# Optimization experiments

Hardware: AMD Instinct MI355X
Metric: run time of the kernel (lower is better)

## Reference

```python
import jax, jax.numpy as jnp
import numpy as np

N = 50000      # nodes
E = 400000     # edges
D = 512        # embed_dim
L = 3          # num gcn layers
INNER = (L + 1) * D
EPS = 1e-5     # BatchNorm1d eps


def setup_inputs() -> dict:
    key = jax.random.key(0)
    ks = jax.random.split(key, 6)
    x = jax.random.normal(ks[0], (N, D), dtype=jnp.float32)
    edge_index = jax.random.randint(ks[1], (2, E), 0, N, dtype=jnp.int64)
    Ws = jax.random.normal(ks[2], (L, D, D), dtype=jnp.float32) / np.float32(np.sqrt(D))
    bs = jnp.zeros((L, D), jnp.float32)
    bn_gamma = jnp.ones((INNER,), jnp.float32)
    bn_beta = jnp.zeros((INNER,), jnp.float32)
    out_W = jax.random.normal(ks[3], (INNER, D), dtype=jnp.float32) / np.float32(np.sqrt(INNER))
    out_b = jnp.zeros((D,), jnp.float32)
    return {"x": x, "edge_index": edge_index, "Ws": Ws, "bs": bs,
            "bn_gamma": bn_gamma, "bn_beta": bn_beta, "out_W": out_W, "out_b": out_b}


def _gcn_conv(x, W, b, src, dst):
    # PyG GCNConv: add self-loops, sym-normalize, aggregate source->target.
    h = x @ W                                            # [N, D]
    deg = jnp.zeros((N,), x.dtype).at[dst].add(1.0) + 1.0  # in-degree + self-loop
    dinv = jax.lax.rsqrt(deg)
    norm = dinv[src] * dinv[dst]                         # [E]
    agg = jnp.zeros_like(h).at[dst].add(h[src] * norm[:, None])
    agg = agg + h * (dinv * dinv)[:, None]               # self-loop messages
    return agg + b


def reference(x, edge_index, Ws, bs, bn_gamma, bn_beta, out_W, out_b):
    src, dst = edge_index[0], edge_index[1]
    h = x
    x_cat = [x]
    for l in range(L):                                   # fixed small layer loop
        h = jax.nn.gelu(_gcn_conv(h, Ws[l], bs[l], src, dst), approximate=False)
        x_cat.append(h)
    xc = jnp.concatenate(x_cat, axis=-1)                 # [N, (L+1)*D]
    # BatchNorm1d, training-mode batch statistics (biased variance)
    mean = jnp.mean(xc, axis=0)
    var = jnp.var(xc, axis=0)
    xn = (xc - mean) * jax.lax.rsqrt(var + EPS) * bn_gamma + bn_beta
    return xn @ out_W + out_b                            # [N, D]
```

## Files before the change

### kernel.cpp

```cpp
#include <hip/hip_runtime.h>
#include <math.h>

#define N_NODES 50000
#define N_EDGES 400000
#define DIM 512
#define NLAYER 3
#define INNER 2048
#define BN_EPS 1e-5f
#define MPAD 50048

typedef unsigned short u16;
typedef unsigned int u32;

typedef __attribute__((ext_vector_type(8))) short bf16x8;
typedef __attribute__((ext_vector_type(4))) float f32x4;

__device__ __forceinline__ u16 f2bf(float f) {
  union { float f; u32 u; } v; v.f = f;
  u32 u = v.u;
  u32 r = (u + 0x7FFFu + ((u >> 16) & 1u)) >> 16;
  return (u16)r;
}
__device__ __forceinline__ float bf2f(u16 h) {
  union { u32 u; float f; } v; v.u = ((u32)h) << 16; return v.f;
}

#define GLOAD_LDS16(g, l)                                                       \
  __builtin_amdgcn_global_load_lds(                                             \
      (const __attribute__((address_space(1))) u32*)(g),                        \
      (__attribute__((address_space(3))) u32*)(l), 16, 0, 0)


__global__ void k_deg(const int* __restrict__ ei, int* __restrict__ deg) {
  int e = blockIdx.x * blockDim.x + threadIdx.x;
  if (e < N_EDGES) atomicAdd(&deg[ei[N_EDGES + e]], 1);
}

__global__ void k_dinv(const int* __restrict__ deg, float* __restrict__ dinv) {
  int i = blockIdx.x * blockDim.x + threadIdx.x;
  if (i < N_NODES) dinv[i] = rsqrtf((float)(deg[i] + 1));
}

__global__ __launch_bounds__(1024) void k_scan(const int* __restrict__ deg,
                                               int* __restrict__ offs, int n) {
  __shared__ int wsum[16];
  __shared__ int carry;
  int tid = threadIdx.x;
  int lane = tid & 63, wv = tid >> 6;
  if (tid == 0) carry = 0;
  __syncthreads();
  for (int base = 0; base < n; base += 1024) {
    int i = base + tid;
    int v = (i < n) ? deg[i] : 0;
    int x = v;
#pragma unroll
    for (int d = 1; d < 64; d <<= 1) {
      int y = __shfl_up(x, d, 64);
      if (lane >= d) x += y;
    }
    if (lane == 63) wsum[wv] = x;
    __syncthreads();
    if (wv == 0) {
      int w = (lane < 16) ? wsum[lane] : 0;
#pragma unroll
      for (int d = 1; d < 16; d <<= 1) {
        int y = __shfl_up(w, d, 64);
        if (lane >= d) w += y;
      }
      if (lane < 16) wsum[lane] = w;
    }
    __syncthreads();
    int prev = carry + (wv ? wsum[wv - 1] : 0);
    if (i < n) offs[i] = prev + x - v;
    int total = wsum[15];
    __syncthreads();
    if (tid == 0) carry += total;
    __syncthreads();
  }
  if (tid == 0) offs[n] = carry;
}

__global__ void k_fill(const int* __restrict__ ei, const int* __restrict__ offs,
                       int* __restrict__ cursor, const float* __restrict__ dinv,
                       int* __restrict__ csr_src, float* __restrict__ csr_norm) {
  int e = blockIdx.x * blockDim.x + threadIdx.x;
  if (e >= N_EDGES) return;
  int s = ei[e];
  int d = ei[N_EDGES + e];
  int p = atomicAdd(&cursor[d], 1);
  int idx = offs[d] + p;
  csr_src[idx] = s;
  csr_norm[idx] = dinv[s] * dinv[d];
}

__global__ void k_convert(const float* __restrict__ src, u16* __restrict__ dst, int n4) {
  int i = blockIdx.x * blockDim.x + threadIdx.x;
  if (i >= n4) return;
  float4 v = ((const float4*)src)[i];
  uint2 o;
  o.x = (u32)f2bf(v.x) | ((u32)f2bf(v.y) << 16);
  o.y = (u32)f2bf(v.z) | ((u32)f2bf(v.w) << 16);
  ((uint2*)dst)[i] = o;
}

__global__ void k_transpose_scale(const float* __restrict__ W, const float* __restrict__ scale,
                                  u16* __restrict__ WT, int K) {
  int t = blockIdx.x * blockDim.x + threadIdx.x;
  if (t >= K * DIM) return;
  int k = t >> 9;
  int j = t & 511;
  float v = W[t];
  if (scale) v *= scale[k];
  WT[(size_t)j * K + k] = f2bf(v);
}

#define BM 128
#define BN 128
#define BK 32

__global__ __launch_bounds__(256) void gemm_bt(
    const u16* __restrict__ A0, const u16* __restrict__ A1,
    const u16* __restrict__ A2, const u16* __restrict__ A3,
    const u16* __restrict__ Bt, const float* __restrict__ bias,
    float* __restrict__ Cf, u16* __restrict__ Cb, int M, int K) {
  __shared__ __align__(16) u16 As[BM * BK];
  __shared__ __align__(16) u16 Bs[BN * BK];
  int tid = threadIdx.x;
  int n0 = blockIdx.x * BN;
  int m0 = blockIdx.y * BM;
  int wave = tid >> 6, lane = tid & 63;
  int wm = (wave & 1) * 64, wn = (wave >> 1) * 64;
  int lr = lane & 15;
  int lq = lane >> 4;

  int ric = lane >> 2;
  int seg = (lane & 3) * 8;

  f32x4 acc[4][4];
#pragma unroll
  for (int i = 0; i < 4; i++)
#pragma unroll
    for (int j = 0; j < 4; j++) acc[i][j] = (f32x4){0.f, 0.f, 0.f, 0.f};

  for (int k0 = 0; k0 < K; k0 += BK) {
    int b = k0 >> 9;
    int kcol = k0 & 511;
    const u16* Abase = (b == 0) ? A0 : (b == 1) ? A1 : (b == 2) ? A2 : A3;
#pragma unroll
    for (int c = 0; c < 2; c++) {
      int chunk = wave * 2 + c;
      int arow = chunk * 16 + ric;
      GLOAD_LDS16(Abase + (size_t)(m0 + arow) * DIM + kcol + seg, &As[chunk * 512]);
      GLOAD_LDS16(Bt + (size_t)(n0 + arow) * K + k0 + seg, &Bs[chunk * 512]);
    }
    __syncthreads();
    bf16x8 af[4], bfr[4];
#pragma unroll
    for (int i = 0; i < 4; i++)
      af[i] = *(const bf16x8*)(&As[(wm + i * 16 + lr) * BK + lq * 8]);
#pragma unroll
    for (int j = 0; j < 4; j++)
      bfr[j] = *(const bf16x8*)(&Bs[(wn + j * 16 + lr) * BK + lq * 8]);
#pragma unroll
    for (int i = 0; i < 4; i++)
#pragma unroll
      for (int j = 0; j < 4; j++)
        acc[i][j] = __builtin_amdgcn_mfma_f32_16x16x32_bf16(af[i], bfr[j], acc[i][j], 0, 0, 0);
    __syncthreads();
  }
#pragma unroll
  for (int i = 0; i < 4; i++) {
    int row_b = m0 + wm + i * 16 + lq * 4;
#pragma unroll
    for (int j = 0; j < 4; j++) {
      int col = n0 + wn + j * 16 + lr;
      float bv = bias ? bias[col] : 0.f;
#pragma unroll
      for (int r = 0; r < 4; r++) {
        int row = row_b + r;
        if (row < M) {
          if (Cf) Cf[(size_t)row * DIM + col] = acc[i][j][r] + bv;
          else    Cb[(size_t)row * DIM + col] = f2bf(acc[i][j][r]);
        }
      }
    }
  }
}

__global__ __launch_bounds__(128) void k_aggregate(
    const u16* __restrict__ hp, const int* __restrict__ offs,
    const int* __restrict__ csr_src, const float* __restrict__ csr_norm,
    const float* __restrict__ dinv, const float* __restrict__ b,
    u16* __restrict__ hb_out) {
  int v = blockIdx.x;
  int c4 = threadIdx.x * 4;
  float4 acc = {0.f, 0.f, 0.f, 0.f};
  int e0 = offs[v], e1 = offs[v + 1];
  for (int e = e0; e < e1; e++) {
    int s = csr_src[e];
    float w = csr_norm[e];
    uint2 hv = *(const uint2*)(hp + (size_t)s * DIM + c4);
    acc.x += w * bf2f((u16)(hv.x & 0xffffu));
    acc.y += w * bf2f((u16)(hv.x >> 16));
    acc.z += w * bf2f((u16)(hv.y & 0xffffu));
    acc.w += w * bf2f((u16)(hv.y >> 16));
  }
  float di = dinv[v];
  float w2 = di * di;
  uint2 hv = *(const uint2*)(hp + (size_t)v * DIM + c4);
  float4 bb = *(const float4*)(b + c4);
  acc.x += w2 * bf2f((u16)(hv.x & 0xffffu)) + bb.x;
  acc.y += w2 * bf2f((u16)(hv.x >> 16)) + bb.y;
  acc.z += w2 * bf2f((u16)(hv.y & 0xffffu)) + bb.z;
  acc.w += w2 * bf2f((u16)(hv.y >> 16)) + bb.w;
  acc.x = 0.5f * acc.x * (1.f + erff(acc.x * 0.70710678118654752f));
  acc.y = 0.5f * acc.y * (1.f + erff(acc.y * 0.70710678118654752f));
  acc.z = 0.5f * acc.z * (1.f + erff(acc.z * 0.70710678118654752f));
  acc.w = 0.5f * acc.w * (1.f + erff(acc.w * 0.70710678118654752f));
  uint2 o;
  o.x = (u32)f2bf(acc.x) | ((u32)f2bf(acc.y) << 16);
  o.y = (u32)f2bf(acc.z) | ((u32)f2bf(acc.w) << 16);
  *(uint2*)(hb_out + (size_t)v * DIM + c4) = o;
}

__global__ void k_bn_stats(const u16* __restrict__ b0, const u16* __restrict__ b1,
                           const u16* __restrict__ b2, const u16* __restrict__ b3,
                           float* __restrict__ sums, float* __restrict__ sumsq,
                           int rows_per) {
  const u16* buf = (blockIdx.x == 0) ? b0 : (blockIdx.x == 1) ? b1 : (blockIdx.x == 2) ? b2 : b3;
  int c = threadIdx.x * 2;
  int col = blockIdx.x * DIM + c;
  int r0 = blockIdx.y * rows_per;
  int r1 = min(N_NODES, r0 + rows_per);
  float s0 = 0.f, ss0 = 0.f, s1 = 0.f, ss1 = 0.f;
  for (int r = r0; r < r1; r++) {
    u32 u = *(const u32*)(buf + (size_t)r * DIM + c);
    float x0 = bf2f((u16)(u & 0xffffu));
    float x1 = bf2f((u16)(u >> 16));
    s0 += x0; ss0 += x0 * x0;
    s1 += x1; ss1 += x1 * x1;
  }
  atomicAdd(&sums[col], s0);
  atomicAdd(&sumsq[col], ss0);
  atomicAdd(&sums[col + 1], s1);
  atomicAdd(&sumsq[col + 1], ss1);
}

__global__ void k_bn_finalize(const float* __restrict__ sums, const float* __restrict__ sumsq,
                              const float* __restrict__ gamma, const float* __restrict__ beta,
                              float* __restrict__ scale, float* __restrict__ shift) {
  int c = blockIdx.x * blockDim.x + threadIdx.x;
  if (c >= INNER) return;
  float mean = sums[c] / (float)N_NODES;
  float var = sumsq[c] / (float)N_NODES - mean * mean;
  float rstd = rsqrtf(var + BN_EPS);
  float sc = gamma[c] * rstd;
  scale[c] = sc;
  shift[c] = beta[c] - mean * sc;
}

__global__ void k_fold_bias(const float* __restrict__ outW, const float* __restrict__ shift,
                            const float* __restrict__ outb, float* __restrict__ biasp) {
  int j = blockIdx.x * blockDim.x + threadIdx.x;
  if (j >= DIM) return;
  float s = 0.f;
  for (int k = 0; k < INNER; k++) s += shift[k] * outW[(size_t)k * DIM + j];
  biasp[j] = s + outb[j];
}

extern "C" void kernel_launch(void* const* d_in, const int* in_sizes, int n_in,
                              void* d_out, int out_size, void* d_ws, size_t ws_size,
                              hipStream_t stream) {
  (void)in_sizes; (void)n_in; (void)out_size; (void)ws_size;
  const float* x     = (const float*)d_in[0];
  const int*   ei    = (const int*)d_in[1];
  const float* Ws    = (const float*)d_in[2];
  const float* bs    = (const float*)d_in[3];
  const float* gamma = (const float*)d_in[4];
  const float* beta  = (const float*)d_in[5];
  const float* outW  = (const float*)d_in[6];
  const float* outb  = (const float*)d_in[7];
  float* out = (float*)d_out;
  u16*   hp  = (u16*)d_out;

  char* ws = (char*)d_ws;
  size_t off = 0;
  auto alloc = [&](size_t bytes) -> void* {
    void* p = ws + off;
    off = (off + bytes + 255) & ~(size_t)255;
    return p;
  };
  int*   deg    = (int*)alloc(N_NODES * 4);
  int*   cursor = (int*)alloc(N_NODES * 4);
  float* sums   = (float*)alloc(INNER * 4);
  float* sumsq  = (float*)alloc(INNER * 4);
  size_t zero_bytes = off;
  float* dinv     = (float*)alloc(N_NODES * 4);
  int*   offs     = (int*)alloc((N_NODES + 1) * 4);
  int*   csr_src  = (int*)alloc(N_EDGES * 4);
  float* csr_norm = (float*)alloc(N_EDGES * 4);
  u16*   xb  = (u16*)alloc((size_t)MPAD * DIM * 2);
  u16*   hb1 = (u16*)alloc((size_t)MPAD * DIM * 2);
  u16*   hb2 = (u16*)alloc((size_t)MPAD * DIM * 2);
  u16*   hb3 = (u16*)alloc((size_t)MPAD * DIM * 2);
  u16*   WbT = (u16*)alloc((size_t)DIM * DIM * 2);
  u16*   WpT = (u16*)alloc((size_t)INNER * DIM * 2);
  float* scale = (float*)alloc(INNER * 4);
  float* shift = (float*)alloc(INNER * 4);
  float* biasp = (float*)alloc(DIM * 4);

  hipMemsetAsync(d_ws, 0, zero_bytes, stream);
  k_deg<<<(N_EDGES + 255) / 256, 256, 0, stream>>>(ei, deg);
  k_dinv<<<(N_NODES + 255) / 256, 256, 0, stream>>>(deg, dinv);
  k_scan<<<1, 1024, 0, stream>>>(deg, offs, N_NODES);
  k_fill<<<(N_EDGES + 255) / 256, 256, 0, stream>>>(ei, offs, cursor, dinv, csr_src, csr_norm);
  k_convert<<<((N_NODES * DIM / 4) + 255) / 256, 256, 0, stream>>>(x, xb, N_NODES * DIM / 4);

  u16* Abufs[4] = {xb, hb1, hb2, hb3};
  dim3 ggrid(DIM / BN, (N_NODES + BM - 1) / BM);
  for (int l = 0; l < NLAYER; l++) {
    k_transpose_scale<<<(DIM * DIM + 255) / 256, 256, 0, stream>>>(
        Ws + (size_t)l * DIM * DIM, nullptr, WbT, DIM);
    const u16* Al = Abufs[l];
    gemm_bt<<<ggrid, 256, 0, stream>>>(Al, Al, Al, Al, WbT, nullptr,
                                       nullptr, hp, N_NODES, DIM);
    k_aggregate<<<N_NODES, 128, 0, stream>>>(hp, offs, csr_src, csr_norm, dinv,
                                             bs + (size_t)l * DIM, Abufs[l + 1]);
  }
  k_bn_stats<<<dim3(4, 125), 256, 0, stream>>>(xb, hb1, hb2, hb3, sums, sumsq, 400);
  k_bn_finalize<<<INNER / 256, 256, 0, stream>>>(sums, sumsq, gamma, beta, scale, shift);
  k_transpose_scale<<<(INNER * DIM + 255) / 256, 256, 0, stream>>>(outW, scale, WpT, INNER);
  k_fold_bias<<<2, 256, 0, stream>>>(outW, shift, outb, biasp);
  gemm_bt<<<ggrid, 256, 0, stream>>>(xb, hb1, hb2, hb3, WpT, biasp,
                                     out, nullptr, N_NODES, INNER);
}
```

Baseline: 1.093 ms.

## Swizzle GEMM tile order and use wave-per-node aggregation with 4-edge unroll

The GEMM now remaps its flat block index into groups of 8 M-tiles that sweep all 4 N-tiles together, so A tiles and the weight matrix are more likely to be reused from L2. The aggregation kernel now assigns one 64-lane wave per node, with each lane loading 16 bytes (8 bf16) per neighbor, and unrolls the edge loop by 4 to keep more gathers in flight. This should cut per-node launch overhead and raise memory-level parallelism for the irregular gathers. Each lane now uses more registers, which may lower occupancy.

After: 1.105 ms. About the same (+1.1%).

```diff
diff --git a/kernel.cpp b/kernel.cpp
--- a/kernel.cpp
+++ b/kernel.cpp
@@ -126,8 +126,18 @@
   __shared__ __align__(16) u16 As[BM * BK];
   __shared__ __align__(16) u16 Bs[BN * BK];
   int tid = threadIdx.x;
-  int n0 = blockIdx.x * BN;
-  int m0 = blockIdx.y * BM;
+
+  int Mblocks = gridDim.y;
+  int flat = blockIdx.y * gridDim.x + blockIdx.x;
+  int g = flat >> 5;
+  int r = flat & 31;
+  int P = Mblocks - (g << 3);
+  P = (P > 8) ? 8 : P;
+  int mb = (g << 3) + r % P;
+  int nb = r / P;
+  int m0 = mb * BM;
+  int n0 = nb * BN;
+
   int wave = tid >> 6, lane = tid & 63;
   int wm = (wave & 1) * 64, wn = (wave >> 1) * 64;
   int lr = lane & 15;
@@ -176,51 +186,77 @@
       int col = n0 + wn + j * 16 + lr;
       float bv = bias ? bias[col] : 0.f;
 #pragma unroll
-      for (int r = 0; r < 4; r++) {
-        int row = row_b + r;
+      for (int r2 = 0; r2 < 4; r2++) {
+        int row = row_b + r2;
         if (row < M) {
-          if (Cf) Cf[(size_t)row * DIM + col] = acc[i][j][r] + bv;
-          else    Cb[(size_t)row * DIM + col] = f2bf(acc[i][j][r]);
+          if (Cf) Cf[(size_t)row * DIM + col] = acc[i][j][r2] + bv;
+          else    Cb[(size_t)row * DIM + col] = f2bf(acc[i][j][r2]);
         }
       }
     }
   }
 }
 
-__global__ __launch_bounds__(128) void k_aggregate(
+__device__ __forceinline__ void accum8(float* a, uint4 h, float w) {
+  a[0] += w * bf2f((u16)(h.x & 0xffffu));
+  a[1] += w * bf2f((u16)(h.x >> 16));
+  a[2] += w * bf2f((u16)(h.y & 0xffffu));
+  a[3] += w * bf2f((u16)(h.y >> 16));
+  a[4] += w * bf2f((u16)(h.z & 0xffffu));
+  a[5] += w * bf2f((u16)(h.z >> 16));
+  a[6] += w * bf2f((u16)(h.w & 0xffffu));
+  a[7] += w * bf2f((u16)(h.w >> 16));
+}
+
+__global__ __launch_bounds__(256) void k_aggregate(
     const u16* __restrict__ hp, const int* __restrict__ offs,
     const int* __restrict__ csr_src, const float* __restrict__ csr_norm,
     const float* __restrict__ dinv, const float* __restrict__ b,
     u16* __restrict__ hb_out) {
-  int v = blockIdx.x;
-  int c4 = threadIdx.x * 4;
-  float4 acc = {0.f, 0.f, 0.f, 0.f};
+  int v = blockIdx.x * 4 + (threadIdx.x >> 6);
+  if (v >= N_NODES) return;
+  int lane = threadIdx.x & 63;
+  int c8 = lane * 8;
+  float acc[8];
+#pragma unroll
+  for (int i = 0; i < 8; i++) acc[i] = 0.f;
+
   int e0 = offs[v], e1 = offs[v + 1];
-  for (int e = e0; e < e1; e++) {
+  int e = e0;
+  for (; e + 4 <= e1; e += 4) {
+    int s0 = csr_src[e], s1 = csr_src[e + 1], s2 = csr_src[e + 2], s3 = csr_src[e + 3];
+    float w0 = csr_norm[e], w1 = csr_norm[e + 1], w2 = csr_norm[e + 2], w3 = csr_norm[e + 3];
+    uint4 h0 = *(const uint4*)(hp + (size_t)s0 * DIM + c8);
+    uint4 h1 = *(const uint4*)(hp + (size_t)s1 * DIM + c8);
+    uint4 h2 = *(const uint4*)(hp + (size_t)s2 * DIM + c8);
+    uint4 h3 = *(const uint4*)(hp + (size_t)s3 * DIM + c8);
+    accum8(acc, h0, w0);
+    accum8(acc, h1, w1);
+    accum8(acc, h2, w2);
+    accum8(acc, h3, w3);
+  }
+  for (; e < e1; e++) {
     int s = csr_src[e];
     float w = csr_norm[e];
-    uint2 hv = *(const uint2*)(hp + (size_t)s * DIM + c4);
-    acc.x += w * bf2f((u16)(hv.x & 0xffffu));
-    acc.y += w * bf2f((u16)(hv.x >> 16));
-    acc.z += w * bf2f((u16)(hv.y & 0xffffu));
-    acc.w += w * bf2f((u16)(hv.y >> 16));
+    uint4 hv = *(const uint4*)(hp + (size_t)s * DIM + c8);
+    accum8(acc, hv, w);
   }
   float di = dinv[v];
-  float w2 = di * di;
-  uint2 hv = *(const uint2*)(hp + (size_t)v * DIM + c4);
-  float4 bb = *(const float4*)(b + c4);
-  acc.x += w2 * bf2f((u16)(hv.x & 0xffffu)) + bb.x;
-  acc.y += w2 * bf2f((u16)(hv.x >> 16)) + bb.y;
-  acc.z += w2 * bf2f((u16)(hv.y & 0xffffu)) + bb.z;
-  acc.w += w2 * bf2f((u16)(hv.y >> 16)) + bb.w;
-  acc.x = 0.5f * acc.x * (1.f + erff(acc.x * 0.70710678118654752f));
-  acc.y = 0.5f * acc.y * (1.f + erff(acc.y * 0.70710678118654752f));
-  acc.z = 0.5f * acc.z * (1.f + erff(acc.z * 0.70710678118654752f));
-  acc.w = 0.5f * acc.w * (1.f + erff(acc.w * 0.70710678118654752f));
-  uint2 o;
-  o.x = (u32)f2bf(acc.x) | ((u32)f2bf(acc.y) << 16);
-  o.y = (u32)f2bf(acc.z) | ((u32)f2bf(acc.w) << 16);
-  *(uint2*)(hb_out + (size_t)v * DIM + c4) = o;
+  uint4 hv = *(const uint4*)(hp + (size_t)v * DIM + c8);
+  accum8(acc, hv, di * di);
+  const float4* bb = (const float4*)(b + c8);
+  float4 b0 = bb[0], b1 = bb[1];
+  acc[0] += b0.x; acc[1] += b0.y; acc[2] += b0.z; acc[3] += b0.w;
+  acc[4] += b1.x; acc[5] += b1.y; acc[6] += b1.z; acc[7] += b1.w;
+#pragma unroll
+  for (int i = 0; i < 8; i++)
+    acc[i] = 0.5f * acc[i] * (1.f + erff(acc[i] * 0.70710678118654752f));
+  uint4 o;
+  o.x = (u32)f2bf(acc[0]) | ((u32)f2bf(acc[1]) << 16);
+  o.y = (u32)f2bf(acc[2]) | ((u32)f2bf(acc[3]) << 16);
+  o.z = (u32)f2bf(acc[4]) | ((u32)f2bf(acc[5]) << 16);
+  o.w = (u32)f2bf(acc[6]) | ((u32)f2bf(acc[7]) << 16);
+  *(uint4*)(hb_out + (size_t)v * DIM + c8) = o;
 }
 
 __global__ void k_bn_stats(const u16* __restrict__ b0, const u16* __restrict__ b1,
@@ -324,8 +360,8 @@
     const u16* Al = Abufs[l];
     gemm_bt<<<ggrid, 256, 0, stream>>>(Al, Al, Al, Al, WbT, nullptr,
                                        nullptr, hp, N_NODES, DIM);
-    k_aggregate<<<N_NODES, 128, 0, stream>>>(hp, offs, csr_src, csr_norm, dinv,
-                                             bs + (size_t)l * DIM, Abufs[l + 1]);
+    k_aggregate<<<(N_NODES + 3) / 4, 256, 0, stream>>>(hp, offs, csr_src, csr_norm, dinv,
+                                                       bs + (size_t)l * DIM, Abufs[l + 1]);
   }
   k_bn_stats<<<dim3(4, 125), 256, 0, stream>>>(xb, hb1, hb2, hb3, sums, sumsq, 400);
   k_bn_finalize<<<INNER / 256, 256, 0, stream>>>(sums, sumsq, gamma, beta, scale, shift);
```
